# Kernel optimization log

Measured on AMD Instinct MI355X. Metric: run time of the kernel, lower is better.

The kernel has to match this reference:

```python
import jax, jax.numpy as jnp
import numpy as np

LENG = 4096
D = 150  # TRANSITION_STATE_OUTPUTS_DIM


def setup_inputs() -> dict:
    key = jax.random.key(0)
    k1, k2 = jax.random.split(key)
    # unweighted adjacency with 2 edge-type channels (values in [0,1) stand in for 0/1 edges)
    adj = jax.random.uniform(k1, (LENG, LENG, 2), dtype=jnp.float32)
    h = jax.random.normal(k2, (LENG, D), dtype=jnp.float32)
    return {"unpreprocessed_unweight_adj_matrix": adj, "h": h}


def reference(unpreprocessed_unweight_adj_matrix, h):
    """Faithful to CalculateHLayer.call:
      h_in[j,d]  = sum_i sum_e adj[i,j,e] * h[i,d]   (reduce over axis 0 and edge axis)
      h_out[i,d] = sum_j sum_e adj[i,j,e] * h[j,d]   (reduce over axis 1 and edge axis)
    Computed without materializing the (L,L,2,D) broadcast: collapse the edge
    axis first, then two GEMMs.
    """
    leng = h.shape[0]
    adj = unpreprocessed_unweight_adj_matrix.reshape(leng, leng, 2)
    A = adj.sum(axis=-1)          # [L, L]
    h_in = jnp.einsum('ij,id->jd', A, h)   # sum over source nodes i
    h_out = jnp.einsum('ij,jd->id', A, h)  # sum over target nodes j
    return (h_in, h_out)
```

## Files before the change

kernel.cpp:

```cpp
#include <hip/hip_runtime.h>


typedef char c16 __attribute__((ext_vector_type(16)));
typedef int i32x4 __attribute__((ext_vector_type(4)));

#define LL 4096
#define DD 150
#define LLDD (LL * DD)
#define BFB ((size_t)10 * 64 * 1024)
#define PB ((size_t)4 * LLDD * 4)
#define AFB ((size_t)256 * 64 * 1024)
#define DEQ (10.0f / 16129.0f)

__global__ __launch_bounds__(256) void prep_kernel(const float* __restrict__ h,
                                                   char* __restrict__ BF) {
    const int lg = blockIdx.x * 256 + threadIdx.x;
    const int u = lg >> 6, l = lg & 63;
    const int nt = u >> 6, S = u & 63;
    const int r = l & 15, g = l >> 4;
    const int d = nt * 16 + r;
    const int j0 = S * 64 + g * 16;
    c16 v;
#pragma unroll
    for (int e = 0; e < 16; ++e) {
        float hv = (d < DD) ? h[(size_t)(j0 + e) * DD + d] : 0.0f;
        int q = (int)rintf(hv * 25.4f);
        q = q < -127 ? -127 : (q > 127 ? 127 : q);
        v[e] = (char)q;
    }
    *(c16*)(BF + (size_t)lg * 16) = v;
}

__global__ __launch_bounds__(256) void convert_kernel(const float* __restrict__ adj,
                                                      char* __restrict__ AF,
                                                      char* __restrict__ ATF) {
    __shared__ __align__(16) char T64[64][80];
    const int tid = threadIdx.x;
    const int bi = blockIdx.x >> 6;
    const int bj = blockIdx.x & 63;
    const float4* adj4 = (const float4*)adj;

#pragma unroll
    for (int it = 0; it < 8; ++it) {
        const int vidx = it * 256 + tid;
        const int il = vidx >> 5, jq = vidx & 31;
        const float4 v = adj4[(size_t)(bi * 64 + il) * 2048 + bj * 32 + jq];
        const int q0 = (int)rintf((v.x + v.y) * 63.5f);
        const int q1 = (int)rintf((v.z + v.w) * 63.5f);
        *(short*)(&T64[il][jq * 2]) = (short)((q0 & 0xff) | ((q1 & 0xff) << 8));
    }
    __syncthreads();

    const int wave = tid >> 6, lane = tid & 63;
    const int r = lane & 15, g = lane >> 4;
    {
        const c16 va = *(const c16*)(&T64[wave * 16 + r][g * 16]);
        *(c16*)(AF + ((size_t)(bi * 4 + wave) * 64 + bj) * 1024 + lane * 16) = va;
    }
    {
        c16 vt;
#pragma unroll
        for (int e = 0; e < 16; ++e) vt[e] = T64[g * 16 + e][wave * 16 + r];
        *(c16*)(ATF + ((size_t)(bj * 4 + wave) * 64 + bi) * 1024 + lane * 16) = vt;
    }
}

__global__ __launch_bounds__(256, 2) void gemm_kernel(const char* __restrict__ AF,
                                                      const char* __restrict__ ATF,
                                                      const char* __restrict__ BF,
                                                      float* __restrict__ P) {
    __shared__ __align__(16) char lds[2][36 * 1024];
    const int tid = threadIdx.x;
    const int wave = tid >> 6, lane = tid & 63;
    const int r = lane & 15, g = lane >> 4;

    const int o = (blockIdx.x & 7) * 64 + (blockIdx.x >> 3);
    const int ks = o & 1;
    const int nh = (o >> 1) & 1;
    const int Mblk = (o >> 2) & 63;
    const int isIn = (o >> 8) & 1;

    const char* Asrc = isIn ? ATF : AF;
    const int T0 = Mblk * 4;
    const int Sbase = ks * 32;

    i32x4 acc[5];
#pragma unroll
    for (int q = 0; q < 5; ++q) acc[q] = (i32x4){0, 0, 0, 0};

#define STAGE(buf, chunkS)                                                           \
    {                                                                                \
        _Pragma("unroll")                                                            \
        for (int k = 0; k < 9; ++k) {                                                \
            const int u = wave * 9 + k;                                              \
            const char* src;                                                         \
            if (u < 16) {                                                            \
                src = Asrc + ((size_t)(T0 + (u >> 2)) * 64 + (chunkS) + (u & 3))     \
                      * 1024;                                                        \
            } else {                                                                 \
                const int v = u - 16;                                                \
                src = BF + ((size_t)(nh * 5 + (v >> 2)) * 64 + (chunkS) + (v & 3))   \
                      * 1024;                                                        \
            }                                                                        \
            __builtin_amdgcn_global_load_lds(                                        \
                (const __attribute__((address_space(1))) void*)(src + lane * 16),    \
                (__attribute__((address_space(3))) void*)(&lds[buf][u * 1024         \
                    + lane * 16]), 16, 0, 0);                                        \
        }                                                                            \
    }

    STAGE(0, Sbase)
    __syncthreads();

    for (int c = 0; c < 8; ++c) {
        const int buf = c & 1;
        if (c < 7) STAGE(buf ^ 1, Sbase + (c + 1) * 4)
        i32x4 a[4];
#pragma unroll
        for (int s = 0; s < 4; ++s)
            a[s] = *(const i32x4*)(&lds[buf][(wave * 4 + s) * 1024 + lane * 16]);
#pragma unroll
        for (int q = 0; q < 5; ++q)
#pragma unroll
            for (int s = 0; s < 4; ++s) {
                const i32x4 b = *(const i32x4*)(&lds[buf][(16 + q * 4 + s) * 1024
                                                          + lane * 16]);
                acc[q] = __builtin_amdgcn_mfma_i32_16x16x64_i8(a[s], b, acc[q],
                                                               0, 0, 0);
            }
        __syncthreads();
    }
#undef STAGE

    float* dst = P + (size_t)(isIn * 2 + ks) * LLDD;
    const int row = (T0 + wave) * 16 + g * 4;
#pragma unroll
    for (int q = 0; q < 5; ++q) {
        const int d = (nh * 5 + q) * 16 + r;
        if (d < DD) {
#pragma unroll
            for (int u = 0; u < 4; ++u)
                dst[(size_t)(row + u) * DD + d] = (float)acc[q][u] * DEQ;
        }
    }
}

__global__ __launch_bounds__(256) void reduce_kernel(const float* __restrict__ P,
                                                     float* __restrict__ out) {
    const int idx = blockIdx.x * 256 + threadIdx.x;
    const int nv = LLDD / 4;
    const float4* p = (const float4*)P;
    const float4* src = (idx < nv) ? (p + (size_t)2 * nv) : p;
    const int e = (idx < nv) ? idx : idx - nv;
    const float4 a = src[e], b = src[e + nv];
    float4 s;
    s.x = a.x + b.x;
    s.y = a.y + b.y;
    s.z = a.z + b.z;
    s.w = a.w + b.w;
    ((float4*)out)[idx] = s;
}

extern "C" void kernel_launch(void* const* d_in, const int* in_sizes, int n_in,
                              void* d_out, int out_size, void* d_ws, size_t ws_size,
                              hipStream_t stream) {
    const float* adj = (const float*)d_in[0];
    const float* h   = (const float*)d_in[1];
    float* out = (float*)d_out;
    char* BF = (char*)d_ws;
    float* P = (float*)((char*)d_ws + BFB);
    char* AF = (char*)d_ws + BFB + PB;
    char* ATF = AF + AFB;

    hipLaunchKernelGGL(prep_kernel, dim3(160), dim3(256), 0, stream, h, BF);
    hipLaunchKernelGGL(convert_kernel, dim3(4096), dim3(256), 0, stream, adj, AF, ATF);
    hipLaunchKernelGGL(gemm_kernel, dim3(512), dim3(256), 0, stream, AF, ATF, BF, P);
    hipLaunchKernelGGL(reduce_kernel, dim3(2 * LLDD / 4 / 256), dim3(256), 0, stream,
                       P, out);
}
```

Measured before the change: 51.24 us.

## Fold h quantization into convert kernel and store split-K partials as fp16

Merges the h-quantization prep kernel into the adjacency convert kernel as 160 extra blocks, removing one kernel launch. Stores the split-K GEMM partial results in fp16 instead of fp32, halving the partial-buffer writes and reads. The reduce kernel now processes 8 halves per thread and upcasts before summing. Rounding the partials to fp16 adds precision loss.

```diff
diff --git a/kernel.cpp b/kernel.cpp
--- a/kernel.cpp
+++ b/kernel.cpp
@@ -3,39 +3,41 @@
 
 typedef char c16 __attribute__((ext_vector_type(16)));
 typedef int i32x4 __attribute__((ext_vector_type(4)));
+typedef _Float16 h8 __attribute__((ext_vector_type(8)));
 
 #define LL 4096
 #define DD 150
 #define LLDD (LL * DD)
 #define BFB ((size_t)10 * 64 * 1024)
-#define PB ((size_t)4 * LLDD * 4)
+#define PB ((size_t)4 * LLDD * 2)
 #define AFB ((size_t)256 * 64 * 1024)
 #define DEQ (10.0f / 16129.0f)
 
-__global__ __launch_bounds__(256) void prep_kernel(const float* __restrict__ h,
-                                                   char* __restrict__ BF) {
-    const int lg = blockIdx.x * 256 + threadIdx.x;
-    const int u = lg >> 6, l = lg & 63;
-    const int nt = u >> 6, S = u & 63;
-    const int r = l & 15, g = l >> 4;
-    const int d = nt * 16 + r;
-    const int j0 = S * 64 + g * 16;
-    c16 v;
-#pragma unroll
-    for (int e = 0; e < 16; ++e) {
-        float hv = (d < DD) ? h[(size_t)(j0 + e) * DD + d] : 0.0f;
-        int q = (int)rintf(hv * 25.4f);
-        q = q < -127 ? -127 : (q > 127 ? 127 : q);
-        v[e] = (char)q;
-    }
-    *(c16*)(BF + (size_t)lg * 16) = v;
-}
-
 __global__ __launch_bounds__(256) void convert_kernel(const float* __restrict__ adj,
+                                                      const float* __restrict__ h,
                                                       char* __restrict__ AF,
-                                                      char* __restrict__ ATF) {
+                                                      char* __restrict__ ATF,
+                                                      char* __restrict__ BF) {
     __shared__ __align__(16) char T64[64][80];
     const int tid = threadIdx.x;
+    if (blockIdx.x >= 4096) {
+        const int lg = (blockIdx.x - 4096) * 256 + tid;
+        const int u = lg >> 6, l = lg & 63;
+        const int nt = u >> 6, S = u & 63;
+        const int r = l & 15, g = l >> 4;
+        const int d = nt * 16 + r;
+        const int j0 = S * 64 + g * 16;
+        c16 v;
+#pragma unroll
+        for (int e = 0; e < 16; ++e) {
+            float hv = (d < DD) ? h[(size_t)(j0 + e) * DD + d] : 0.0f;
+            int q = (int)rintf(hv * 25.4f);
+            q = q < -127 ? -127 : (q > 127 ? 127 : q);
+            v[e] = (char)q;
+        }
+        *(c16*)(BF + (size_t)lg * 16) = v;
+        return;
+    }
     const int bi = blockIdx.x >> 6;
     const int bj = blockIdx.x & 63;
     const float4* adj4 = (const float4*)adj;
@@ -68,7 +70,7 @@
 __global__ __launch_bounds__(256, 2) void gemm_kernel(const char* __restrict__ AF,
                                                       const char* __restrict__ ATF,
                                                       const char* __restrict__ BF,
-                                                      float* __restrict__ P) {
+                                                      _Float16* __restrict__ P) {
     __shared__ __align__(16) char lds[2][36 * 1024];
     const int tid = threadIdx.x;
     const int wave = tid >> 6, lane = tid & 63;
@@ -132,7 +134,7 @@
     }
 #undef STAGE
 
-    float* dst = P + (size_t)(isIn * 2 + ks) * LLDD;
+    _Float16* dst = P + (size_t)(isIn * 2 + ks) * LLDD;
     const int row = (T0 + wave) * 16 + g * 4;
 #pragma unroll
     for (int q = 0; q < 5; ++q) {
@@ -140,25 +142,30 @@
         if (d < DD) {
 #pragma unroll
             for (int u = 0; u < 4; ++u)
-                dst[(size_t)(row + u) * DD + d] = (float)acc[q][u] * DEQ;
+                dst[(size_t)(row + u) * DD + d] = (_Float16)((float)acc[q][u] * DEQ);
         }
     }
 }
 
-__global__ __launch_bounds__(256) void reduce_kernel(const float* __restrict__ P,
+__global__ __launch_bounds__(256) void reduce_kernel(const _Float16* __restrict__ P,
                                                      float* __restrict__ out) {
     const int idx = blockIdx.x * 256 + threadIdx.x;
-    const int nv = LLDD / 4;
-    const float4* p = (const float4*)P;
-    const float4* src = (idx < nv) ? (p + (size_t)2 * nv) : p;
+    const int nv = LLDD / 8;
+    const _Float16* src = (idx < nv) ? (P + (size_t)2 * LLDD) : P;
     const int e = (idx < nv) ? idx : idx - nv;
-    const float4 a = src[e], b = src[e + nv];
-    float4 s;
-    s.x = a.x + b.x;
-    s.y = a.y + b.y;
-    s.z = a.z + b.z;
-    s.w = a.w + b.w;
-    ((float4*)out)[idx] = s;
+    const h8 a = *(const h8*)(src + (size_t)e * 8);
+    const h8 b = *(const h8*)(src + (size_t)LLDD + (size_t)e * 8);
+    float4 s0, s1;
+    s0.x = (float)a[0] + (float)b[0];
+    s0.y = (float)a[1] + (float)b[1];
+    s0.z = (float)a[2] + (float)b[2];
+    s0.w = (float)a[3] + (float)b[3];
+    s1.x = (float)a[4] + (float)b[4];
+    s1.y = (float)a[5] + (float)b[5];
+    s1.z = (float)a[6] + (float)b[6];
+    s1.w = (float)a[7] + (float)b[7];
+    ((float4*)out)[idx * 2] = s0;
+    ((float4*)out)[idx * 2 + 1] = s1;
 }
 
 extern "C" void kernel_launch(void* const* d_in, const int* in_sizes, int n_in,
@@ -168,13 +175,13 @@
     const float* h   = (const float*)d_in[1];
     float* out = (float*)d_out;
     char* BF = (char*)d_ws;
-    float* P = (float*)((char*)d_ws + BFB);
+    _Float16* P = (_Float16*)((char*)d_ws + BFB);
     char* AF = (char*)d_ws + BFB + PB;
     char* ATF = AF + AFB;
 
-    hipLaunchKernelGGL(prep_kernel, dim3(160), dim3(256), 0, stream, h, BF);
-    hipLaunchKernelGGL(convert_kernel, dim3(4096), dim3(256), 0, stream, adj, AF, ATF);
+    hipLaunchKernelGGL(convert_kernel, dim3(4256), dim3(256), 0, stream,
+                       adj, h, AF, ATF, BF);
     hipLaunchKernelGGL(gemm_kernel, dim3(512), dim3(256), 0, stream, AF, ATF, BF, P);
-    hipLaunchKernelGGL(reduce_kernel, dim3(2 * LLDD / 4 / 256), dim3(256), 0, stream,
+    hipLaunchKernelGGL(reduce_kernel, dim3(2 * LLDD / 8 / 256), dim3(256), 0, stream,
                        P, out);
 }
```

New measurement: 46.61 us. 9.0% less time.
